# Performance work log

Hardware: AMD Instinct MI355X
Metric: run time of the kernel (lower is better)

Reference implementation:

```python
import jax, jax.numpy as jnp
import numpy as np


def setup_inputs() -> dict:
    key = jax.random.key(0)
    k1, k2, k3 = jax.random.split(key, 3)
    N, C, H, W = 4, 64, 256, 448
    img = jax.random.normal(k1, (N, C, H, W), dtype=jnp.float32)
    flow = jax.random.normal(k2, (N, 2, H, W), dtype=jnp.float32)
    z = jax.random.normal(k3, (N, 1, H, W), dtype=jnp.float32)
    return {"img": img, "flow": flow, "z": z}


def _splat(prepared, flow):
    # prepared: [N, C1, H, W], flow: [N, 2, H, W]
    N, C1, H, W = prepared.shape
    dtype = prepared.dtype
    gy, gx = jnp.meshgrid(jnp.arange(H, dtype=dtype), jnp.arange(W, dtype=dtype), indexing="ij")
    fx = gx[None] + flow[:, 0]  # [N, H, W]
    fy = gy[None] + flow[:, 1]
    finite = jnp.isfinite(fx) & jnp.isfinite(fy)
    sx = jnp.where(finite, fx, 0.0)
    sy = jnp.where(finite, fy, 0.0)
    x0 = jnp.floor(sx)
    y0 = jnp.floor(sy)
    x1 = x0 + 1.0
    y1 = y0 + 1.0
    x0i = x0.astype(jnp.int32)
    y0i = y0.astype(jnp.int32)
    x1i = x1.astype(jnp.int32)
    y1i = y1.astype(jnp.int32)
    # bilinear weights per corner
    w00 = (x1 - sx) * (y1 - sy)
    w10 = (sx - x0) * (y1 - sy)
    w01 = (x1 - sx) * (sy - y0)
    w11 = (sx - x0) * (sy - y0)
    inx0 = (x0i >= 0) & (x0i < W)
    inx1 = (x1i >= 0) & (x1i < W)
    iny0 = (y0i >= 0) & (y0i < H)
    iny1 = (y1i >= 0) & (y1i < H)
    m00 = finite & inx0 & iny0
    m10 = finite & inx1 & iny0
    m01 = finite & inx0 & iny1
    m11 = finite & inx1 & iny1
    x0c = jnp.clip(x0i, 0, W - 1)
    x1c = jnp.clip(x1i, 0, W - 1)
    y0c = jnp.clip(y0i, 0, H - 1)
    y1c = jnp.clip(y1i, 0, H - 1)
    base = (jnp.arange(N, dtype=jnp.int32) * (H * W))[:, None, None]  # [N,1,1]
    idx = jnp.stack([
        base + y0c * W + x0c,
        base + y0c * W + x1c,
        base + y1c * W + x0c,
        base + y1c * W + x1c,
    ], 0).reshape(4, -1)  # [4, N*H*W]
    w = jnp.stack([
        w00 * m00.astype(dtype),
        w10 * m10.astype(dtype),
        w01 * m01.astype(dtype),
        w11 * m11.astype(dtype),
    ], 0).reshape(4, -1)  # [4, N*H*W]
    feats = prepared.transpose(0, 2, 3, 1).reshape(-1, C1)  # [N*H*W, C1]
    values = (feats[None] * w[:, :, None]).reshape(-1, C1)  # [4*N*H*W, C1]
    out = jnp.zeros((N * H * W, C1), dtype=dtype).at[idx.reshape(-1)].add(values)
    return out.reshape(N, H, W, C1).transpose(0, 3, 1, 2)


def reference(img, flow, z):
    # strType='softmax' -> mode 'soft-zeroeps'
    metric_exp = jnp.exp(z)  # [N,1,H,W]
    prepared = jnp.concatenate([img * metric_exp, metric_exp], axis=1)
    out = _splat(prepared, flow)
    norm = out[:, -1:, :, :]
    norm = jnp.where(norm == 0.0, jnp.ones_like(norm), norm)
    return out[:, :-1, :, :] / norm
```

## Files before the change

kernel.cpp:

```cpp
#include <hip/hip_runtime.h>
#include <hip/hip_fp16.h>
#include <cmath>

#define NN 4
#define CC 64
#define HH 256
#define WW 448
#define HW (HH * WW)
#define CHW (CC * HW)

#define TW 32
#define TH 16
#define TPX (TW * TH)
#define RADI 4
#define RGW (TW + 2 * RADI)
#define RGH (TH + 2 * RADI)
#define RPX (RGW * RGH)
#define NTX (WW / TW)
#define NTY (HH / TH)
#define CAP 12
#define G 4
#define NG (CC / G)
#define SIDECAP 64
#define OVCAP 8192

struct __align__(16) OvEntry { int n, p, x0, y0; float w00, w10, w01, w11; };

__global__ __launch_bounds__(256) void fallback_kernel(
    const float* __restrict__ flow, const float* __restrict__ z, int* __restrict__ ov)
{
    const int gid = blockIdx.x * 256 + threadIdx.x;
    const int n = gid / HW;
    const int p = gid - n * HW;
    const int gy = p / WW;
    const int gx = p - gy * WW;
    const float fl0 = flow[(size_t)(n * 2 + 0) * HW + p];
    const float fl1 = flow[(size_t)(n * 2 + 1) * HW + p];
    if (!(isfinite(fl0) && isfinite(fl1))) return;
    if (fabsf(fl0) <= (float)RADI && fabsf(fl1) <= (float)RADI) return;
    const float sx = (float)gx + fl0, sy = (float)gy + fl1;
    const float x0f = floorf(sx), y0f = floorf(sy);
    const int x0 = (int)x0f, y0 = (int)y0f;
    const float wx1 = sx - x0f, wx0 = 1.0f - wx1;
    const float wy1 = sy - y0f, wy0 = 1.0f - wy1;
    const float me = expf(z[(size_t)n * HW + p]);
    const bool inx0 = (x0 >= 0) & (x0 < WW);
    const bool inx1 = (x0 + 1 >= 0) & (x0 + 1 < WW);
    const bool iny0 = (y0 >= 0) & (y0 < HH);
    const bool iny1 = (y0 + 1 >= 0) & (y0 + 1 < HH);
    OvEntry e;
    e.n = n; e.p = p; e.x0 = x0; e.y0 = y0;
    e.w00 = (inx0 && iny0) ? wx0 * wy0 * me : 0.0f;
    e.w10 = (inx1 && iny0) ? wx1 * wy0 * me : 0.0f;
    e.w01 = (inx0 && iny1) ? wx0 * wy1 * me : 0.0f;
    e.w11 = (inx1 && iny1) ? wx1 * wy1 * me : 0.0f;
    if (e.w00 == 0.0f && e.w10 == 0.0f && e.w01 == 0.0f && e.w11 == 0.0f) return;
    const int idx = atomicAdd(ov, 1);
    if (idx < OVCAP) ((OvEntry*)(ov + 8))[idx] = e;
}

__global__ __launch_bounds__(512, 6) void gather_kernel(
    const float* __restrict__ img,
    const float* __restrict__ flow,
    const float* __restrict__ z,
    float* __restrict__ out,
    const int* __restrict__ ov)
{
    __shared__ __align__(16) float s_u[RPX * G];
    __shared__ unsigned s_pk[TPX * CAP];
    __shared__ unsigned s_cnt[TPX];
    __shared__ unsigned s_sm[SIDECAP];
    __shared__ float s_sw[SIDECAP];
    __shared__ int s_scnt;

    const int bid = blockIdx.x;
    const int n = bid / (NTX * NTY);
    const int t = bid - n * (NTX * NTY);
    const int tx = (t % NTX) * TW;
    const int ty = (t / NTX) * TH;
    const int tid = threadIdx.x;

    s_cnt[tid] = 0u;
    if (tid == 0) s_scnt = 0;
    __syncthreads();

    const float* fxp = flow + (size_t)(n * 2 + 0) * HW;
    const float* fyp = flow + (size_t)(n * 2 + 1) * HW;
    const float* zp  = z + (size_t)n * HW;

    for (int it = 0; it < 2; ++it) {
        const int idx = it * 512 + tid;
        if (idx < RPX) {
            const int ry = idx / RGW, rx = idx - ry * RGW;
            const int gx = tx - RADI + rx;
            const int gy = ty - RADI + ry;
            if (gx >= 0 && gx < WW && gy >= 0 && gy < HH) {
                const int p = gy * WW + gx;
                const float fl0 = fxp[p], fl1 = fyp[p];
                if (isfinite(fl0) && isfinite(fl1) &&
                    fabsf(fl0) <= (float)RADI && fabsf(fl1) <= (float)RADI) {
                    const float sx = (float)gx + fl0, sy = (float)gy + fl1;
                    const float x0f = floorf(sx), y0f = floorf(sy);
                    const int x0 = (int)x0f, y0 = (int)y0f;
                    const float wx1 = sx - x0f, wx0 = 1.0f - wx1;
                    const float wy1 = sy - y0f, wy0 = 1.0f - wy1;
                    const float me = expf(zp[p]);
#pragma unroll
                    for (int cy = 0; cy < 2; ++cy) {
#pragma unroll
                        for (int cx = 0; cx < 2; ++cx) {
                            const int px = x0 + cx - tx;
                            const int py = y0 + cy - ty;
                            if (px >= 0 && px < TW && py >= 0 && py < TH) {
                                const float w = (cx ? wx1 : wx0) * (cy ? wy1 : wy0) * me;
                                const unsigned short hb =
                                    __half_as_ushort(__float2half(w));
                                if (hb) {
                                    const int pix = py * TW + px;
                                    const unsigned slot = atomicAdd(&s_cnt[pix], 1u);
                                    if (slot < CAP) {
                                        s_pk[pix * CAP + slot] =
                                            (unsigned)idx | ((unsigned)hb << 16);
                                    } else {
                                        const int si = atomicAdd(&s_scnt, 1);
                                        if (si < SIDECAP) {
                                            s_sm[si] = (unsigned)pix | ((unsigned)idx << 16);
                                            s_sw[si] = __half2float(__ushort_as_half(hb));
                                        }
                                    }
                                }
                            }
                        }
                    }
                }
            }
        }
    }

    int ovcnt = ov[0];
    ovcnt = ovcnt > OVCAP ? OVCAP : ovcnt;
    const OvEntry* oe = (const OvEntry*)(ov + 8);
    for (int i = tid; i < ovcnt; i += 512) {
        const OvEntry e = oe[i];
        if (e.n != n) continue;
        const float ws[4] = { e.w00, e.w10, e.w01, e.w11 };
#pragma unroll
        for (int cy = 0; cy < 2; ++cy) {
#pragma unroll
            for (int cx = 0; cx < 2; ++cx) {
                const int px = e.x0 + cx - tx;
                const int py = e.y0 + cy - ty;
                const float w = ws[cy * 2 + cx];
                if (px >= 0 && px < TW && py >= 0 && py < TH && w != 0.0f) {
                    const int si = atomicAdd(&s_scnt, 1);
                    if (si < SIDECAP) {
                        s_sm[si] = (unsigned)(py * TW + px) | ((unsigned)(1024 + i) << 16);
                        s_sw[si] = w;
                    }
                }
            }
        }
    }
    __syncthreads();

    const unsigned kraw = s_cnt[tid];
    const int k = kraw < CAP ? (int)kraw : CAP;
    int rli[CAP];
    float rlw[CAP];
    float norm = 0.0f;
#pragma unroll
    for (int j = 0; j < CAP; ++j) {
        const unsigned pk = (j < k) ? s_pk[tid * CAP + j] : 0u;
        rli[j] = (int)(pk & 0xFFFFu);
        const float w = __half2float(__ushort_as_half((unsigned short)(pk >> 16)));
        rlw[j] = w;
        norm += w;
    }
    int scnt = s_scnt; scnt = scnt > SIDECAP ? SIDECAP : scnt;
    for (int s = 0; s < scnt; ++s)
        if ((int)(s_sm[s] & 0xFFFFu) == tid) norm += s_sw[s];
    const float rnorm = (norm == 0.0f) ? 1.0f : 1.0f / norm;

    const int rgy0 = ty - RADI, rgx0 = tx - RADI;
    const int j0 = tid, j1 = tid + 512;
    const int ry0_ = j0 / RGW, rx0_ = j0 - ry0_ * RGW;
    const int ry1_ = j1 / RGW, rx1_ = j1 - ry1_ * RGW;
    const int gX0 = rgx0 + rx0_, gY0 = rgy0 + ry0_;
    const int gX1 = rgx0 + rx1_, gY1 = rgy0 + ry1_;
    const bool ok0 = (gX0 >= 0) & (gX0 < WW) & (gY0 >= 0) & (gY0 < HH);
    const bool ok1 = (j1 < RPX) & (gX1 >= 0) & (gX1 < WW) & (gY1 >= 0) & (gY1 < HH);
    const int po0 = gY0 * WW + gX0;
    const int po1 = gY1 * WW + gX1;

    const int lx = tid & (TW - 1);
    const int ly = tid >> 5;
    const float* imgn = img + (size_t)n * CHW;
    float* outn = out + (size_t)n * CHW;
    const int qp = (ty + ly) * WW + tx + lx;

    float rv0[G], rv1[G];
    auto prefetch = [&](int g) {
        const float* bp = imgn + g * (G * HW);
#pragma unroll
        for (int c = 0; c < G; ++c) {
            rv0[c] = ok0 ? bp[c * HW + po0] : 0.0f;
            rv1[c] = ok1 ? bp[c * HW + po1] : 0.0f;
        }
    };

    prefetch(0);
    for (int g = 0; g < NG; ++g) {
        __syncthreads();
#pragma unroll
        for (int c = 0; c < G; ++c) s_u[c * RPX + j0] = rv0[c];
        if (j1 < RPX) {
#pragma unroll
            for (int c = 0; c < G; ++c) s_u[c * RPX + j1] = rv1[c];
        }
        __syncthreads();
        if (g + 1 < NG) prefetch(g + 1);

        float acc0 = 0.0f, acc1 = 0.0f, acc2 = 0.0f, acc3 = 0.0f;
#pragma unroll
        for (int j = 0; j < CAP; ++j) {
            if (j >= k) break;
            const int ri = rli[j];
            const float w = rlw[j];
            acc0 += w * s_u[0 * RPX + ri];
            acc1 += w * s_u[1 * RPX + ri];
            acc2 += w * s_u[2 * RPX + ri];
            acc3 += w * s_u[3 * RPX + ri];
        }

        for (int s = 0; s < scnt; ++s) {
            const unsigned sm = s_sm[s];
            if ((int)(sm & 0xFFFFu) != tid) continue;
            const int code = (int)(sm >> 16);
            const float w = s_sw[s];
            if (code < 1024) {
                acc0 += w * s_u[0 * RPX + code];
                acc1 += w * s_u[1 * RPX + code];
                acc2 += w * s_u[2 * RPX + code];
                acc3 += w * s_u[3 * RPX + code];
            } else {
                const float* ap = imgn + g * (G * HW) + oe[code - 1024].p;
                acc0 += w * ap[0 * HW];
                acc1 += w * ap[1 * HW];
                acc2 += w * ap[2 * HW];
                acc3 += w * ap[3 * HW];
            }
        }

        float* op = outn + g * (G * HW) + qp;
        op[0 * HW] = acc0 * rnorm;
        op[1 * HW] = acc1 * rnorm;
        op[2 * HW] = acc2 * rnorm;
        op[3 * HW] = acc3 * rnorm;
    }
}

extern "C" void kernel_launch(void* const* d_in, const int* in_sizes, int n_in,
                              void* d_out, int out_size, void* d_ws, size_t ws_size,
                              hipStream_t stream) {
    const float* img  = (const float*)d_in[0];
    const float* flow = (const float*)d_in[1];
    const float* z    = (const float*)d_in[2];
    float* out = (float*)d_out;
    int* ov = (int*)d_ws;

    hipMemsetAsync(d_ws, 0, 32, stream);
    fallback_kernel<<<(NN * HW) / 256, 256, 0, stream>>>(flow, z, ov);
    gather_kernel<<<NN * NTX * NTY, 512, 0, stream>>>(img, flow, z, out, ov);
}
```

Baseline: 277.4 us.

## Double-buffer halo tile in LDS and load image with float4

The per-group image halo is now loaded with 16-byte float4 global loads, each thread fetching four consecutive pixels of one channel instead of four scalar loads across channels. The halo is double-buffered in shared memory by reusing the s_pk array, which is dead after the per-thread weights are read into registers, as the second buffer. This cuts the loop from two barriers per group to one and lets staging for the next group overlap compute on the current one. It relies on s_pk being large enough for a full buffer and on the halo column offsets keeping the float4 accesses aligned.

```diff
diff --git a/kernel.cpp b/kernel.cpp
--- a/kernel.cpp
+++ b/kernel.cpp
@@ -21,6 +21,9 @@
 #define CAP 12
 #define G 4
 #define NG (CC / G)
+#define PLANE RPX
+#define BUFSZ (RPX * G)
+#define F4PP 240
 #define SIDECAP 64
 #define OVCAP 8192
 
@@ -66,8 +69,8 @@
     float* __restrict__ out,
     const int* __restrict__ ov)
 {
-    __shared__ __align__(16) float s_u[RPX * G];
-    __shared__ unsigned s_pk[TPX * CAP];
+    __shared__ __align__(16) float s_a[BUFSZ];
+    __shared__ __align__(16) unsigned s_pk[TPX * CAP];
     __shared__ unsigned s_cnt[TPX];
     __shared__ unsigned s_sm[SIDECAP];
     __shared__ float s_sw[SIDECAP];
@@ -181,16 +184,19 @@
         if ((int)(s_sm[s] & 0xFFFFu) == tid) norm += s_sw[s];
     const float rnorm = (norm == 0.0f) ? 1.0f : 1.0f / norm;
 
-    const int rgy0 = ty - RADI, rgx0 = tx - RADI;
-    const int j0 = tid, j1 = tid + 512;
-    const int ry0_ = j0 / RGW, rx0_ = j0 - ry0_ * RGW;
-    const int ry1_ = j1 / RGW, rx1_ = j1 - ry1_ * RGW;
-    const int gX0 = rgx0 + rx0_, gY0 = rgy0 + ry0_;
-    const int gX1 = rgx0 + rx1_, gY1 = rgy0 + ry1_;
-    const bool ok0 = (gX0 >= 0) & (gX0 < WW) & (gY0 >= 0) & (gY0 < HH);
-    const bool ok1 = (j1 < RPX) & (gX1 >= 0) & (gX1 < WW) & (gY1 >= 0) & (gY1 < HH);
-    const int po0 = gY0 * WW + gX0;
-    const int po1 = gY1 * WW + gX1;
+    const int q0 = tid, q1 = tid + 512;
+    const int c0 = q0 / F4PP, r0 = q0 - c0 * F4PP;
+    const int row0 = r0 / 10, col0 = (r0 - row0 * 10) * 4;
+    const int c1 = q1 / F4PP, r1 = q1 - c1 * F4PP;
+    const int row1 = r1 / 10, col1 = (r1 - row1 * 10) * 4;
+    const int gyA = ty - RADI + row0, gxA = tx - RADI + col0;
+    const int gyB = ty - RADI + row1, gxB = tx - RADI + col1;
+    const bool okA = (gyA >= 0) & (gyA < HH) & (gxA >= 0) & (gxA < WW);
+    const bool okB = (q1 < RPX) & (gyB >= 0) & (gyB < HH) & (gxB >= 0) & (gxB < WW);
+    const int poA = gyA * WW + gxA;
+    const int poB = gyB * WW + gxB;
+    const int ldsA = c0 * PLANE + row0 * RGW + col0;
+    const int ldsB = c1 * PLANE + row1 * RGW + col1;
 
     const int lx = tid & (TW - 1);
     const int ly = tid >> 5;
@@ -198,26 +204,25 @@
     float* outn = out + (size_t)n * CHW;
     const int qp = (ty + ly) * WW + tx + lx;
 
-    float rv0[G], rv1[G];
+    float4 pv0, pv1;
     auto prefetch = [&](int g) {
-        const float* bp = imgn + g * (G * HW);
-#pragma unroll
-        for (int c = 0; c < G; ++c) {
-            rv0[c] = ok0 ? bp[c * HW + po0] : 0.0f;
-            rv1[c] = ok1 ? bp[c * HW + po1] : 0.0f;
-        }
+        pv0 = okA ? *(const float4*)(imgn + (g * G + c0) * HW + poA)
+                  : make_float4(0.f, 0.f, 0.f, 0.f);
+        pv1 = okB ? *(const float4*)(imgn + (g * G + c1) * HW + poB)
+                  : make_float4(0.f, 0.f, 0.f, 0.f);
     };
+    float* bufB = (float*)s_pk;
+    auto stage = [&](float* buf) {
+        *(float4*)(buf + ldsA) = pv0;
+        if (q1 < RPX) *(float4*)(buf + ldsB) = pv1;
+    };
 
     prefetch(0);
+    stage(s_a);
+    __syncthreads();
+    float* cur = s_a;
+    float* nxt = bufB;
     for (int g = 0; g < NG; ++g) {
-        __syncthreads();
-#pragma unroll
-        for (int c = 0; c < G; ++c) s_u[c * RPX + j0] = rv0[c];
-        if (j1 < RPX) {
-#pragma unroll
-            for (int c = 0; c < G; ++c) s_u[c * RPX + j1] = rv1[c];
-        }
-        __syncthreads();
         if (g + 1 < NG) prefetch(g + 1);
 
         float acc0 = 0.0f, acc1 = 0.0f, acc2 = 0.0f, acc3 = 0.0f;
@@ -226,10 +231,10 @@
             if (j >= k) break;
             const int ri = rli[j];
             const float w = rlw[j];
-            acc0 += w * s_u[0 * RPX + ri];
-            acc1 += w * s_u[1 * RPX + ri];
-            acc2 += w * s_u[2 * RPX + ri];
-            acc3 += w * s_u[3 * RPX + ri];
+            acc0 += w * cur[0 * PLANE + ri];
+            acc1 += w * cur[1 * PLANE + ri];
+            acc2 += w * cur[2 * PLANE + ri];
+            acc3 += w * cur[3 * PLANE + ri];
         }
 
         for (int s = 0; s < scnt; ++s) {
@@ -238,10 +243,10 @@
             const int code = (int)(sm >> 16);
             const float w = s_sw[s];
             if (code < 1024) {
-                acc0 += w * s_u[0 * RPX + code];
-                acc1 += w * s_u[1 * RPX + code];
-                acc2 += w * s_u[2 * RPX + code];
-                acc3 += w * s_u[3 * RPX + code];
+                acc0 += w * cur[0 * PLANE + code];
+                acc1 += w * cur[1 * PLANE + code];
+                acc2 += w * cur[2 * PLANE + code];
+                acc3 += w * cur[3 * PLANE + code];
             } else {
                 const float* ap = imgn + g * (G * HW) + oe[code - 1024].p;
                 acc0 += w * ap[0 * HW];
@@ -256,6 +261,10 @@
         op[1 * HW] = acc1 * rnorm;
         op[2 * HW] = acc2 * rnorm;
         op[3 * HW] = acc3 * rnorm;
+
+        if (g + 1 < NG) stage(nxt);
+        __syncthreads();
+        float* tmp = cur; cur = nxt; nxt = tmp;
     }
 }
 
```

Result: no change. 272.6 us (-1.7%).
